# Optimization experiments

Hardware: AMD Instinct MI355X
Metric: run time of the kernel (lower is better)

Reference implementation:

```python
import jax, jax.numpy as jnp
import numpy as np

RADIUS = 0.15
NSAMPLE = 128
NPOINT = 128
EPS = 1e-5  # BatchNorm eps (eval mode, running_mean=0, running_var=1)


def _bn(x, g, b):
    shape = (1, -1) + (1,) * (x.ndim - 2)
    return x * (g / jnp.sqrt(1.0 + EPS)).reshape(shape) + b.reshape(shape)


def _fps(x, npoint):
    # farthest point sampling; x: (Bk, N, 3) -> (Bk, npoint) int32
    Bn, N, _ = x.shape

    def step(carry, _):
        dist, far = carry
        c = jnp.take_along_axis(x, far[:, None, None], 1)  # (Bk,1,3)
        d = jnp.sum((x - c) ** 2, -1)
        dist = jnp.minimum(dist, d)
        return (dist, jnp.argmax(dist, -1).astype(jnp.int32)), far

    init = (jnp.full((Bn, N), 1e10, x.dtype), jnp.zeros((Bn,), jnp.int32))
    _, idxs = jax.lax.scan(step, init, None, length=npoint)
    return idxs.T  # (Bk, npoint)


def _sa_module(x, f, mlp):
    # PointnetSAModuleVotes: FPS -> ball query -> group (use_xyz, normalize_xyz)
    # -> shared MLP (conv2d 1x1 + BN + ReLU) -> max over nsample.
    Bk, M, _ = x.shape
    fps_idx = _fps(x, NPOINT)
    new_xyz = jnp.take_along_axis(x, fps_idx[..., None], 1)  # (Bk,np,3)
    d2 = jnp.sum((new_xyz[:, :, None, :] - x[:, None, :, :]) ** 2, -1)  # (Bk,np,M)
    cand = jnp.where(d2 < RADIUS ** 2, jnp.arange(M)[None, None, :], M)
    cand = jnp.sort(cand, -1)[..., :NSAMPLE]  # first nsample in-radius indices
    first = cand[..., :1]
    first = jnp.where(first == M, 0, first)
    idx = jnp.where(cand == M, first, cand)  # (Bk,np,ns), pad with first valid
    gx = jnp.take_along_axis(x, idx.reshape(Bk, -1)[..., None], 1).reshape(Bk, NPOINT, NSAMPLE, 3)
    gxn = (gx - new_xyz[:, :, None, :]) / RADIUS  # normalize_xyz=True
    gf = jnp.take_along_axis(f[:, :, None, :], idx[:, None, :, :], 3)  # (Bk,C,np,ns)
    h = jnp.concatenate([gxn.transpose(0, 3, 1, 2), gf], 1)  # (Bk, C+3, np, ns)
    for (w, b, g, be) in mlp:
        h = jax.nn.relu(_bn(jnp.einsum('oc,bcps->bops', w, h) + b[None, :, None, None], g, be))
    return new_xyz, h.max(-1)  # (Bk,np,3), (Bk,128,np)


def setup_inputs() -> dict:
    key = jax.random.key(0)
    ks = iter(jax.random.split(key, 40))
    B, M, K, C = 2, 1024, 19, 256
    inp = {}
    inp['xyz'] = jax.random.normal(next(ks), (B, M, K, 3), jnp.float32)
    inp['features'] = jax.random.normal(next(ks), (B, C, K, M), jnp.float32)

    def conv_p(prefix, cin, cout):
        inp[prefix + '_w'] = jax.random.normal(next(ks), (cout, cin), jnp.float32) * (1.0 / np.sqrt(cin))
        inp[prefix + '_b'] = jax.random.normal(next(ks), (cout,), jnp.float32) * 0.02
        inp[prefix + '_g'] = 1.0 + 0.1 * jax.random.normal(next(ks), (cout,), jnp.float32)
        inp[prefix + '_be'] = 0.02 * jax.random.normal(next(ks), (cout,), jnp.float32)

    conv_p('m1', C + 3, 128)  # use_xyz -> 259 in-channels
    conv_p('m2', 128, 128)
    conv_p('m3', 128, 128)
    conv_p('c1', 128, 128)
    conv_p('c2', 128, 128)
    inp['op_w'] = jax.random.normal(next(ks), (K, 5, 128), jnp.float32) * (1.0 / np.sqrt(128))
    inp['op_b'] = jax.random.normal(next(ks), (K, 5), jnp.float32) * 0.02
    return inp


def reference(xyz, features, m1_w, m1_b, m1_g, m1_be, m2_w, m2_b, m2_g, m2_be,
              m3_w, m3_b, m3_g, m3_be, c1_w, c1_b, c1_g, c1_be,
              c2_w, c2_b, c2_g, c2_be, op_w, op_b):
    B, M, K, _ = xyz.shape
    C = features.shape[1]
    # fold vote_factor k into the batch dim (all per-k SA/conv weights are shared)
    x = xyz.transpose(0, 2, 1, 3).reshape(B * K, M, 3)
    f = features.transpose(0, 2, 1, 3).reshape(B * K, C, M)
    mlp = [(m1_w, m1_b, m1_g, m1_be), (m2_w, m2_b, m2_g, m2_be), (m3_w, m3_b, m3_g, m3_be)]
    new_xyz, feat = _sa_module(x, f, mlp)
    net = jax.nn.relu(_bn(jnp.einsum('oc,bcp->bop', c1_w, feat) + c1_b[None, :, None], c1_g, c1_be))
    net = jax.nn.relu(_bn(jnp.einsum('oc,bcp->bop', c2_w, net) + c2_b[None, :, None], c2_g, c2_be))
    net = net.reshape(B, K, 128, NPOINT)
    # per-k output conv (conv_op ModuleList), 128 -> 2+3
    out = jnp.einsum('koc,bkcp->bkop', op_w, net) + op_b[None, :, :, None]
    net_t = out.transpose(0, 1, 3, 2)  # (B,K,np,5)
    agg_xyz = new_xyz.reshape(B, K, NPOINT, 3)
    center = agg_xyz + net_t[..., 2:5]  # decode_scores_
    scores = jnp.concatenate([net_t[..., :2], center], -1)  # obj(2) + center(3)
    return scores, agg_xyz, feat.reshape(B, K, 128, NPOINT)
```

## Files before the change

kernel.cpp:

```cpp
#include <hip/hip_runtime.h>
#include <math.h>

#define NBK   38

#define OFF_XC    0u
#define OFF_NXYZ  466944u
#define OFF_BIDX  525312u
#define OFF_W1F   3015680u
#define OFF_PREP  22938624u
#define OFF_WF    22955008u
#define OFF_CNT   23348224u

#define OUT_AGG   24320
#define OUT_FEAT  38912

typedef short bf16x8 __attribute__((ext_vector_type(8)));
typedef float f32x4  __attribute__((ext_vector_type(4)));
typedef int   v4i    __attribute__((ext_vector_type(4)));
typedef int   v2i    __attribute__((ext_vector_type(2)));

__device__ __forceinline__ float dist2f(float a0, float a1, float a2,
                                        float b0, float b1, float b2) {
#pragma clang fp contract(off)
  float d0 = a0 - b0;
  float d1 = a1 - b1;
  float d2 = a2 - b2;
  return d0 * d0 + d1 * d1 + d2 * d2;
}

__device__ __forceinline__ void split2rn(float v, unsigned& sh, unsigned& sm) {
  unsigned u = __float_as_uint(v);
  unsigned rh = (u + 0x7fffu + ((u >> 16) & 1u)) & 0xffff0000u;
  sh = rh >> 16;
  float r1 = v - __uint_as_float(rh);
  unsigned u1 = __float_as_uint(r1);
  unsigned rm = (u1 + 0x7fffu + ((u1 >> 16) & 1u)) & 0xffff0000u;
  sm = rm >> 16;
}

__global__ __launch_bounds__(1024, 4) void front_kernel(
    const float* __restrict__ xyz, const float* __restrict__ feats,
    const float* __restrict__ m1w, const float* __restrict__ m1b,
    const float* __restrict__ m1g, const float* __restrict__ m1be,
    const float* __restrict__ m2w, const float* __restrict__ m2b,
    const float* __restrict__ m2g, const float* __restrict__ m2be,
    const float* __restrict__ m3w, const float* __restrict__ m3b,
    const float* __restrict__ m3g, const float* __restrict__ m3be,
    const float* __restrict__ c1w, const float* __restrict__ c1b,
    const float* __restrict__ c1g, const float* __restrict__ c1be,
    const float* __restrict__ c2w, const float* __restrict__ c2b,
    const float* __restrict__ c2g, const float* __restrict__ c2be,
    float* __restrict__ xc, float* __restrict__ nxyz, float* __restrict__ agg,
    int* __restrict__ bidx, int* __restrict__ counts,
    float* __restrict__ W1f, short* __restrict__ Wf, float* __restrict__ prep)
{
  __shared__ __align__(16) char smem[32768];
  int bid = blockIdx.x, t = threadIdx.x;
  int wave = t >> 6, lane = t & 63;

  if (bid < NBK) {
    int bk = bid;
    int b = bk / 19, k = bk % 19;
    float* sx0 = (float*)smem;
    float* sx1 = sx0 + 1024;
    float* sx2 = sx1 + 1024;
    float* sp0 = sx2 + 1024;
    float* sp1 = sp0 + 1088;
    float* sp2 = sp1 + 1088;
    float* scen = sp2 + 1088;

    const float* src = xyz + ((size_t)((b * 1024 + t) * 19 + k)) * 3;
    float x0 = src[0], x1 = src[1], x2 = src[2];
    sx0[t] = x0; sx1[t] = x1; sx2[t] = x2;
    int tp = t + (t >> 4);
    sp0[tp] = x0; sp1[tp] = x1; sp2[tp] = x2;
    xc[(bk * 3 + 0) * 1024 + t] = x0;
    xc[(bk * 3 + 1) * 1024 + t] = x1;
    xc[(bk * 3 + 2) * 1024 + t] = x2;
    __syncthreads();

    if (wave == 0) {
      float px[16], py[16], pz[16], dist[16];
      int base = lane * 17;
#pragma unroll
      for (int j = 0; j < 16; ++j) {
        px[j] = sp0[base + j];
        py[j] = sp1[base + j];
        pz[j] = sp2[base + j];
        dist[j] = 1e10f;
      }
      int far = 0;
      for (int it = 0; it < 128; ++it) {
        int fa = far + (far >> 4);
        float c0 = sp0[fa], c1 = sp1[fa], c2 = sp2[fa];
        if (lane == 0) {
          scen[it * 3 + 0] = c0;
          scen[it * 3 + 1] = c1;
          scen[it * 3 + 2] = c2;
        }
#pragma unroll
        for (int j = 0; j < 16; ++j) {
          float d = dist2f(px[j], py[j], pz[j], c0, c1, c2);
          dist[j] = fminf(dist[j], d);
        }
        float tv[8]; int tj[8];
#pragma unroll
        for (int i = 0; i < 8; ++i) {
          bool L = dist[2 * i] >= dist[2 * i + 1];
          tv[i] = L ? dist[2 * i] : dist[2 * i + 1];
          tj[i] = L ? (2 * i) : (2 * i + 1);
        }
#pragma unroll
        for (int s = 1; s < 8; s <<= 1) {
#pragma unroll
          for (int i = 0; i < 8; i += 2 * s) {
            bool L = tv[i] >= tv[i + s];
            tv[i] = L ? tv[i] : tv[i + s];
            tj[i] = L ? tj[i] : tj[i + s];
          }
        }
        float lmax = tv[0];
        float g = lmax;
#pragma unroll
        for (int off = 1; off <= 32; off <<= 1)
          g = fmaxf(g, __shfl_xor(g, off));
        unsigned long long mk = __ballot(lmax == g);
        int wl = __builtin_ctzll(mk);
        far = __shfl((lane << 4) + tj[0], wl);
      }
    }
    __syncthreads();

    if (t < 384) {
      float v = scen[t];
      nxyz[bk * 384 + t] = v;
      agg[bk * 384 + t]  = v;
    }

    for (int p = wave * 8; p < wave * 8 + 8; ++p) {
      float c0 = scen[p * 3 + 0], c1 = scen[p * 3 + 1], c2 = scen[p * 3 + 2];
      int* outp = bidx + ((size_t)(bk * 128 + p)) * 128;
      int count = 0, first = 0;
      bool got = false;
      for (int ch = 0; ch < 16 && count < 128; ++ch) {
        int m = (ch << 6) + lane;
        float d = dist2f(sx0[m], sx1[m], sx2[m], c0, c1, c2);
        bool flag = d < 0.0225f;
        unsigned long long mask = __ballot(flag);
        if (!got && mask) { first = (ch << 6) + __builtin_ctzll(mask); got = true; }
        int pos = count + (int)__popcll(mask & ((1ull << lane) - 1ull));
        if (flag && pos < 128) outp[pos] = m;
        count += (int)__popcll(mask);
      }
      for (int j = count + lane; j < 128; j += 64) outp[j] = first;
      if (lane == 0) counts[bk * 128 + p] = count > 128 ? 128 : count;
    }
    return;
  }

  if (bid < 342) {
    short* ffrag = (short*)smem;
    if (t >= 256) {
      for (int i = 0; i < 8; ++i) __syncthreads();
      return;
    }
    int blk = bid - NBK;
    int bk = blk >> 3, m0 = (blk & 7) << 7;
    int b = bk / 19, k = bk % 19;
    int quad = lane >> 4, nl = lane & 15;
    int mloc = t & 127, chalf = t >> 7;
    int st_w = mloc >> 4, sl_w = mloc & 15;
    const float* fbase = feats + ((size_t)(b * 4864 + k)) * 1024 + m0 + mloc;

    f32x4 acc[2][8];
#pragma unroll
    for (int oi = 0; oi < 2; ++oi)
#pragma unroll
      for (int st = 0; st < 8; ++st) acc[oi][st] = (f32x4){0.f, 0.f, 0.f, 0.f};

    for (int ch = 0; ch < 4; ++ch) {
      int cbase = ch * 64 + chalf * 32;
#pragma unroll
      for (int g = 0; g < 4; ++g) {
        float v[8];
#pragma unroll
        for (int j = 0; j < 8; ++j)
          v[j] = fbase[(size_t)(cbase + g * 8 + j) * 19456];
        unsigned sh[8], sm[8];
#pragma unroll
        for (int j = 0; j < 8; ++j) split2rn(v[j], sh[j], sm[j]);
        int base = chalf * 4096 + st_w * 512 + (g * 16 + sl_w) * 8;
        v4i ph = {(int)(sh[0] | (sh[1] << 16)), (int)(sh[2] | (sh[3] << 16)),
                  (int)(sh[4] | (sh[5] << 16)), (int)(sh[6] | (sh[7] << 16))};
        *(v4i*)&ffrag[base] = ph;
        v4i pm = {(int)(sm[0] | (sm[1] << 16)), (int)(sm[2] | (sm[3] << 16)),
                  (int)(sm[4] | (sm[5] << 16)), (int)(sm[6] | (sm[7] << 16))};
        *(v4i*)&ffrag[base + 8192] = pm;
      }
      __syncthreads();
#pragma unroll
      for (int kkl = 0; kkl < 2; ++kkl) {
        int kk = ch * 2 + kkl;
        bf16x8 a[2][2];
#pragma unroll
        for (int oi = 0; oi < 2; ++oi) {
          int o_row = (wave * 2 + oi) * 16 + nl;
          const float* wsrc = m1w + o_row * 259 + 3 + kk * 32 + quad * 8;
          float wv[8];
#pragma unroll
          for (int j = 0; j < 8; ++j) wv[j] = wsrc[j];
          unsigned sh[8], sm[8];
#pragma unroll
          for (int j = 0; j < 8; ++j) split2rn(wv[j], sh[j], sm[j]);
          short ah[8], am[8];
#pragma unroll
          for (int j = 0; j < 8; ++j) { ah[j] = (short)sh[j]; am[j] = (short)sm[j]; }
          a[oi][0] = (bf16x8){ah[0], ah[1], ah[2], ah[3], ah[4], ah[5], ah[6], ah[7]};
          a[oi][1] = (bf16x8){am[0], am[1], am[2], am[3], am[4], am[5], am[6], am[7]};
        }
#pragma unroll
        for (int st = 0; st < 8; ++st) {
          const short* hb = ffrag + kkl * 4096 + st * 512 + lane * 8;
          bf16x8 b0 = *(const bf16x8*)hb;
          bf16x8 b1 = *(const bf16x8*)(hb + 8192);
#pragma unroll
          for (int oi = 0; oi < 2; ++oi) {
            f32x4 c = acc[oi][st];
            c = __builtin_amdgcn_mfma_f32_16x16x32_bf16(a[oi][1], b0, c, 0, 0, 0);
            c = __builtin_amdgcn_mfma_f32_16x16x32_bf16(a[oi][0], b1, c, 0, 0, 0);
            c = __builtin_amdgcn_mfma_f32_16x16x32_bf16(a[oi][0], b0, c, 0, 0, 0);
            acc[oi][st] = c;
          }
        }
      }
      __syncthreads();
    }
    float inv = 1.0f / sqrtf(1.0f + 1e-5f);
#pragma unroll
    for (int oi = 0; oi < 2; ++oi) {
      int o0 = (wave * 2 + oi) * 16 + quad * 4;
      float4 bb = *(const float4*)&m1b[o0];
      float4 gg = *(const float4*)&m1g[o0];
#pragma unroll
      for (int st = 0; st < 8; ++st) {
        int m_out = m0 + st * 16 + nl;
        f32x4 cc = acc[oi][st];
        float4 r;
        r.x = (cc[0] + bb.x) * (gg.x * inv);
        r.y = (cc[1] + bb.y) * (gg.y * inv);
        r.z = (cc[2] + bb.z) * (gg.z * inv);
        r.w = (cc[3] + bb.w) * (gg.w * inv);
        *(float4*)&W1f[((size_t)(bk * 1024 + m_out)) * 128 + o0] = r;
      }
    }
    return;
  }

  if (bid < 350) {
    int idx = (bid - 342) * 1024 + t;
#pragma unroll
    for (int e = 0; e < 4; ++e) {
      int i = idx * 4 + e;
      int c = i & 127, o = (i >> 7) & 127, l = i >> 14;
      float w = (l ? m3w : m2w)[o * 128 + c];
      unsigned sh, sm;
      split2rn(w, sh, sm);
      int ot = o >> 4, mm = o & 15, kk = c >> 5, q = (c & 31) >> 3, j = c & 7;
      int within = (q * 16 + mm) * 8 + j;
      Wf[(((l * 2 + 0) * 4 + kk) * 8 + ot) * 512 + within] = (short)sh;
      Wf[(((l * 2 + 1) * 4 + kk) * 8 + ot) * 512 + within] = (short)sm;
    }
    return;
  }

  if (bid < 358) {
    int idx2 = (bid - 350) * 1024 + t;
#pragma unroll
    for (int e = 0; e < 4; ++e) {
      int i = idx2 * 4 + e;
      int c = i & 127, o = (i >> 7) & 127, l = i >> 14;
      float w = (l ? c2w : c1w)[o * 128 + c];
      unsigned sh, sm;
      split2rn(w, sh, sm);
      int ot = o >> 4, mm = o & 15, kk = c >> 5, q = (c & 31) >> 3, j = c & 7;
      int within = (q * 16 + mm) * 8 + j;
      Wf[131072 + (((l * 2 + 0) * 4 + kk) * 8 + ot) * 512 + within] = (short)sh;
      Wf[131072 + (((l * 2 + 1) * 4 + kk) * 8 + ot) * 512 + within] = (short)sm;
    }
    return;
  }

  if (t < 128) {
    float inv = 1.0f / sqrtf(1.0f + 1e-5f);
    float a1 = m1g[t] * inv;
    prep[t] = a1;
    float a2 = m2g[t] * inv;  prep[256 + t] = a2;  prep[384 + t] = fmaf(m2b[t], a2, m2be[t]);
    float a3 = m3g[t] * inv;  prep[512 + t] = a3;  prep[640 + t] = fmaf(m3b[t], a3, m3be[t]);
    float ac1 = c1g[t] * inv; prep[768 + t] = ac1; prep[896 + t] = fmaf(c1b[t], ac1, c1be[t]);
    float ac2 = c2g[t] * inv; prep[1024 + t] = ac2; prep[1152 + t] = fmaf(c2b[t], ac2, c2be[t]);
    prep[1280 + 4 * t + 0] = m1w[t * 259 + 0] * a1;
    prep[1280 + 4 * t + 1] = m1w[t * 259 + 1] * a1;
    prep[1280 + 4 * t + 2] = m1w[t * 259 + 2] * a1;
    prep[1280 + 4 * t + 3] = m1be[t];
  }
}

__device__ __forceinline__ void mfma_layer(const short* __restrict__ Wf,
                                           const short* hfrag, int l,
                                           int wave, int lane, int nst_h,
                                           f32x4 acc[2][4])
{
#pragma unroll 1
  for (int kk = 0; kk < 4; ++kk) {
    bf16x8 a[2][2];
#pragma unroll
    for (int oi = 0; oi < 2; ++oi)
#pragma unroll
      for (int sp = 0; sp < 2; ++sp)
        a[oi][sp] = *(const bf16x8*)(Wf + (((l * 2 + sp) * 4 + kk) * 8 + (wave * 2 + oi)) * 512 + lane * 8);
    for (int st = 0; st < nst_h; ++st) {
      const short* hb = hfrag + kk * 2048 + st * 512 + lane * 8;
      bf16x8 b0 = *(const bf16x8*)(hb);
      bf16x8 b1 = *(const bf16x8*)(hb + 8192);
#pragma unroll
      for (int oi = 0; oi < 2; ++oi) {
        f32x4 c = acc[oi][st];
        c = __builtin_amdgcn_mfma_f32_16x16x32_bf16(a[oi][1], b0, c, 0, 0, 0);
        c = __builtin_amdgcn_mfma_f32_16x16x32_bf16(a[oi][0], b1, c, 0, 0, 0);
        c = __builtin_amdgcn_mfma_f32_16x16x32_bf16(a[oi][0], b0, c, 0, 0, 0);
        acc[oi][st] = c;
      }
    }
  }
}

__global__ __launch_bounds__(256, 3) void sa_kernel(
    const float* __restrict__ xc, const float* __restrict__ nxyz,
    const int* __restrict__ bidx, const int* __restrict__ counts,
    const float* __restrict__ W1f, const float* __restrict__ prep,
    const short* __restrict__ Wf, float* __restrict__ feat_out)
{
  __shared__ __align__(16) short hfrag[16384];
  __shared__ float pcs[512];
  __shared__ float sm[32 * 128];
  __shared__ float ccen[12];
  __shared__ int scnt[4];
  int gb = blockIdx.x, bk = gb >> 5, pb = (gb & 31) << 2;
  int t = threadIdx.x;
  int wave = t >> 6, lane = t & 63;
  int quad = lane >> 4, nl = lane & 15;

  pcs[t] = prep[1280 + t];
  pcs[256 + t] = prep[1536 + t];
  if (t < 4) scnt[t] = counts[bk * 128 + pb + t];
  if (t < 12) {
    int bb = t / 3, c = t % 3;
    ccen[t] = nxyz[(bk * 128 + pb + bb) * 3 + c];
  }
  __syncthreads();
  int n0 = (scnt[0] + 15) >> 4, n1 = (scnt[1] + 15) >> 4;
  int n2 = (scnt[2] + 15) >> 4, n3 = (scnt[3] + 15) >> 4;
  int pf1 = n0, pf2 = n0 + n1, pf3 = n0 + n1 + n2, T = n0 + n1 + n2 + n3;

  for (int q0 = 0; q0 < T; q0 += 4) {
    int nst_h = T - q0;
    if (nst_h > 4) nst_h = 4;
    {
      int cg = wave;
      int st = lane >> 4, sl = lane & 15;
      if (st < nst_h) {
        int q = q0 + st;
        int bq = (q >= pf1) + (q >= pf2) + (q >= pf3);
        int tstart = (bq == 0) ? 0 : (bq == 1) ? pf1 : (bq == 2) ? pf2 : pf3;
        int tslot = q - tstart;
        int m = bidx[((size_t)(bk * 128 + pb + bq)) * 128 + tslot * 16 + sl];
        float cen0 = ccen[bq * 3 + 0], cen1 = ccen[bq * 3 + 1], cen2 = ccen[bq * 3 + 2];
        float g0 = (xc[(bk * 3 + 0) * 1024 + m] - cen0) * (1.0f / 0.15f);
        float g1 = (xc[(bk * 3 + 1) * 1024 + m] - cen1) * (1.0f / 0.15f);
        float g2 = (xc[(bk * 3 + 2) * 1024 + m] - cen2) * (1.0f / 0.15f);
        const float4* wrow = (const float4*)(W1f + ((size_t)(bk * 1024 + m)) * 128 + cg * 32);
        const float4* pcp = (const float4*)pcs + cg * 32;
#pragma unroll
        for (int g = 0; g < 4; ++g) {
          float4 wva = wrow[g * 2], wvb = wrow[g * 2 + 1];
          float wv[8] = {wva.x, wva.y, wva.z, wva.w, wvb.x, wvb.y, wvb.z, wvb.w};
          unsigned sh[8], smv[8];
#pragma unroll
          for (int e = 0; e < 8; ++e) {
            float4 pc = pcp[g * 8 + e];
            float hv = fmaxf(wv[e] + pc.x * g0 + pc.y * g1 + pc.z * g2 + pc.w, 0.f);
            split2rn(hv, sh[e], smv[e]);
          }
          int base = (cg * 4 + st) * 512 + (g * 16 + sl) * 8;
          v4i ph = {(int)(sh[0] | (sh[1] << 16)), (int)(sh[2] | (sh[3] << 16)),
                    (int)(sh[4] | (sh[5] << 16)), (int)(sh[6] | (sh[7] << 16))};
          *(v4i*)&hfrag[base] = ph;
          v4i pm = {(int)(smv[0] | (smv[1] << 16)), (int)(smv[2] | (smv[3] << 16)),
                    (int)(smv[4] | (smv[5] << 16)), (int)(smv[6] | (smv[7] << 16))};
          *(v4i*)&hfrag[base + 8192] = pm;
        }
      }
    }
    __syncthreads();

    f32x4 acc[2][4];
#pragma unroll
    for (int oi = 0; oi < 2; ++oi)
#pragma unroll
      for (int st = 0; st < 4; ++st) acc[oi][st] = (f32x4){0.f, 0.f, 0.f, 0.f};
    mfma_layer(Wf, hfrag, 0, wave, lane, nst_h, acc);
    __syncthreads();

#pragma unroll
    for (int oi = 0; oi < 2; ++oi) {
      int o0 = (wave * 2 + oi) * 16 + quad * 4;
      float4 al = *(const float4*)&prep[256 + o0];
      float4 be = *(const float4*)&prep[384 + o0];
      int kk2 = o0 >> 5, g2 = (o0 & 31) >> 3, j0 = o0 & 7;
      for (int st = 0; st < nst_h; ++st) {
        f32x4 cc = acc[oi][st];
        float v0 = fmaxf(fmaf(cc[0], al.x, be.x), 0.f);
        float v1 = fmaxf(fmaf(cc[1], al.y, be.y), 0.f);
        float v2 = fmaxf(fmaf(cc[2], al.z, be.z), 0.f);
        float v3 = fmaxf(fmaf(cc[3], al.w, be.w), 0.f);
        unsigned h0, m0_, h1, m1_, h2, m2_, h3, m3_;
        split2rn(v0, h0, m0_); split2rn(v1, h1, m1_);
        split2rn(v2, h2, m2_); split2rn(v3, h3, m3_);
        int base = (kk2 * 4 + st) * 512 + (g2 * 16 + nl) * 8 + j0;
        v2i w0 = {(int)(h0 | (h1 << 16)), (int)(h2 | (h3 << 16))};
        *(v2i*)&hfrag[base] = w0;
        v2i w1 = {(int)(m0_ | (m1_ << 16)), (int)(m2_ | (m3_ << 16))};
        *(v2i*)&hfrag[base + 8192] = w1;
      }
    }
    __syncthreads();

#pragma unroll
    for (int oi = 0; oi < 2; ++oi)
#pragma unroll
      for (int st = 0; st < 4; ++st) acc[oi][st] = (f32x4){0.f, 0.f, 0.f, 0.f};
    mfma_layer(Wf, hfrag, 1, wave, lane, nst_h, acc);

#pragma unroll
    for (int oi = 0; oi < 2; ++oi) {
      int o0 = (wave * 2 + oi) * 16 + quad * 4;
      float4 al = *(const float4*)&prep[512 + o0];
      float4 be = *(const float4*)&prep[640 + o0];
      for (int st = 0; st < nst_h; ++st) {
        f32x4 cc = acc[oi][st];
        float v[4];
        v[0] = fmaxf(fmaf(cc[0], al.x, be.x), 0.f);
        v[1] = fmaxf(fmaf(cc[1], al.y, be.y), 0.f);
        v[2] = fmaxf(fmaf(cc[2], al.z, be.z), 0.f);
        v[3] = fmaxf(fmaf(cc[3], al.w, be.w), 0.f);
#pragma unroll
        for (int r = 0; r < 4; ++r) {
          float x = v[r];
          x = fmaxf(x, __shfl_xor(x, 1));
          x = fmaxf(x, __shfl_xor(x, 2));
          x = fmaxf(x, __shfl_xor(x, 4));
          x = fmaxf(x, __shfl_xor(x, 8));
          if (nl == 0) sm[(q0 + st) * 128 + o0 + r] = x;
        }
      }
    }
    __syncthreads();
  }

#pragma unroll
  for (int e = t; e < 512; e += 256) {
    int bb = e >> 7, o = e & 127;
    int qs = (bb == 0) ? 0 : (bb == 1) ? pf1 : (bb == 2) ? pf2 : pf3;
    int nq = (bb == 0) ? n0 : (bb == 1) ? n1 : (bb == 2) ? n2 : n3;
    float v = sm[qs * 128 + o];
    for (int q = 1; q < nq; ++q) v = fmaxf(v, sm[(qs + q) * 128 + o]);
    feat_out[(((size_t)bk) << 14) + (o << 7) + pb + bb] = v;
  }
}

__global__ __launch_bounds__(256) void head_kernel(const float* __restrict__ featg,
    const float* __restrict__ prep, const short* __restrict__ Wf,
    const float* __restrict__ nxyz, const float* __restrict__ opw,
    const float* __restrict__ opb, float* __restrict__ scores)
{
  __shared__ __align__(16) short hfrag[16384];
  __shared__ float hplain[128 * 65];
  int bk = blockIdx.x >> 1, p0 = (blockIdx.x & 1) << 6;
  int t = threadIdx.x;
  int wave = t >> 6, lane = t & 63;
  int quad = lane >> 4, nl = lane & 15;
  const short* WC = Wf + 131072;

  {
    int cg = wave;
    int st = lane >> 4, sl = lane & 15;
    const float* fb = featg + (bk << 14) + p0 + lane;
#pragma unroll
    for (int g = 0; g < 4; ++g) {
      float v[8];
#pragma unroll
      for (int e = 0; e < 8; ++e)
        v[e] = fb[(cg * 32 + g * 8 + e) << 7];
      unsigned sh[8], sm[8];
#pragma unroll
      for (int e = 0; e < 8; ++e) split2rn(v[e], sh[e], sm[e]);
      int base = (cg * 4 + st) * 512 + (g * 16 + sl) * 8;
      v4i ph = {(int)(sh[0] | (sh[1] << 16)), (int)(sh[2] | (sh[3] << 16)),
                (int)(sh[4] | (sh[5] << 16)), (int)(sh[6] | (sh[7] << 16))};
      *(v4i*)&hfrag[base] = ph;
      v4i pm = {(int)(sm[0] | (sm[1] << 16)), (int)(sm[2] | (sm[3] << 16)),
                (int)(sm[4] | (sm[5] << 16)), (int)(sm[6] | (sm[7] << 16))};
      *(v4i*)&hfrag[base + 8192] = pm;
    }
  }
  __syncthreads();

  f32x4 acc[2][4];
#pragma unroll
  for (int oi = 0; oi < 2; ++oi)
#pragma unroll
    for (int st = 0; st < 4; ++st) acc[oi][st] = (f32x4){0.f, 0.f, 0.f, 0.f};
  mfma_layer(WC, hfrag, 0, wave, lane, 4, acc);
  __syncthreads();

#pragma unroll
  for (int oi = 0; oi < 2; ++oi) {
    int o0 = (wave * 2 + oi) * 16 + quad * 4;
    float4 al = *(const float4*)&prep[768 + o0];
    float4 be = *(const float4*)&prep[896 + o0];
    int kk2 = o0 >> 5, g2 = (o0 & 31) >> 3, j0 = o0 & 7;
#pragma unroll
    for (int st = 0; st < 4; ++st) {
      f32x4 cc = acc[oi][st];
      float v0 = fmaxf(fmaf(cc[0], al.x, be.x), 0.f);
      float v1 = fmaxf(fmaf(cc[1], al.y, be.y), 0.f);
      float v2 = fmaxf(fmaf(cc[2], al.z, be.z), 0.f);
      float v3 = fmaxf(fmaf(cc[3], al.w, be.w), 0.f);
      unsigned h0, m0_, h1, m1_, h2, m2_, h3, m3_;
      split2rn(v0, h0, m0_); split2rn(v1, h1, m1_);
      split2rn(v2, h2, m2_); split2rn(v3, h3, m3_);
      int base = (kk2 * 4 + st) * 512 + (g2 * 16 + nl) * 8 + j0;
      v2i w0 = {(int)(h0 | (h1 << 16)), (int)(h2 | (h3 << 16))};
      *(v2i*)&hfrag[base] = w0;
      v2i w1 = {(int)(m0_ | (m1_ << 16)), (int)(m2_ | (m3_ << 16))};
      *(v2i*)&hfrag[base + 8192] = w1;
    }
  }
  __syncthreads();

#pragma unroll
  for (int oi = 0; oi < 2; ++oi)
#pragma unroll
    for (int st = 0; st < 4; ++st) acc[oi][st] = (f32x4){0.f, 0.f, 0.f, 0.f};
  mfma_layer(WC, hfrag, 1, wave, lane, 4, acc);

#pragma unroll
  for (int oi = 0; oi < 2; ++oi) {
    int o0 = (wave * 2 + oi) * 16 + quad * 4;
    float4 al = *(const float4*)&prep[1024 + o0];
    float4 be = *(const float4*)&prep[1152 + o0];
#pragma unroll
    for (int st = 0; st < 4; ++st) {
      f32x4 cc = acc[oi][st];
      int p = st * 16 + nl;
      hplain[(o0 + 0) * 65 + p] = fmaxf(fmaf(cc[0], al.x, be.x), 0.f);
      hplain[(o0 + 1) * 65 + p] = fmaxf(fmaf(cc[1], al.y, be.y), 0.f);
      hplain[(o0 + 2) * 65 + p] = fmaxf(fmaf(cc[2], al.z, be.z), 0.f);
      hplain[(o0 + 3) * 65 + p] = fmaxf(fmaf(cc[3], al.w, be.w), 0.f);
    }
  }
  __syncthreads();

  if (t < 64) {
    int p = t, k = bk % 19;
    float res[5];
#pragma unroll
    for (int j = 0; j < 5; ++j) {
      const float* wr = opw + ((size_t)(k * 5 + j)) * 128;
      float a = opb[k * 5 + j];
      for (int c = 0; c < 128; ++c) a = fmaf(wr[c], hplain[c * 65 + p], a);
      res[j] = a;
    }
    int pg = p0 + p;
    float a0 = nxyz[(bk * 128 + pg) * 3 + 0];
    float a1 = nxyz[(bk * 128 + pg) * 3 + 1];
    float a2 = nxyz[(bk * 128 + pg) * 3 + 2];
    float* sc = scores + ((size_t)(bk * 128 + pg)) * 5;
    sc[0] = res[0];
    sc[1] = res[1];
    sc[2] = a0 + res[2];
    sc[3] = a1 + res[3];
    sc[4] = a2 + res[4];
  }
}

extern "C" void kernel_launch(void* const* d_in, const int* in_sizes, int n_in,
                              void* d_out, int out_size, void* d_ws, size_t ws_size,
                              hipStream_t stream) {
  (void)in_sizes; (void)n_in; (void)out_size; (void)ws_size;
  const float* xyz  = (const float*)d_in[0];
  const float* fts  = (const float*)d_in[1];
  const float* m1w  = (const float*)d_in[2];
  const float* m1b  = (const float*)d_in[3];
  const float* m1g  = (const float*)d_in[4];
  const float* m1be = (const float*)d_in[5];
  const float* m2w  = (const float*)d_in[6];
  const float* m2b  = (const float*)d_in[7];
  const float* m2g  = (const float*)d_in[8];
  const float* m2be = (const float*)d_in[9];
  const float* m3w  = (const float*)d_in[10];
  const float* m3b  = (const float*)d_in[11];
  const float* m3g  = (const float*)d_in[12];
  const float* m3be = (const float*)d_in[13];
  const float* c1w  = (const float*)d_in[14];
  const float* c1b  = (const float*)d_in[15];
  const float* c1g  = (const float*)d_in[16];
  const float* c1be = (const float*)d_in[17];
  const float* c2w  = (const float*)d_in[18];
  const float* c2b  = (const float*)d_in[19];
  const float* c2g  = (const float*)d_in[20];
  const float* c2be = (const float*)d_in[21];
  const float* opw  = (const float*)d_in[22];
  const float* opb  = (const float*)d_in[23];

  float* out = (float*)d_out;
  char* ws = (char*)d_ws;
  float* xc   = (float*)(ws + OFF_XC);
  float* nxyz = (float*)(ws + OFF_NXYZ);
  int*   bidx = (int*)(ws + OFF_BIDX);
  float* W1f  = (float*)(ws + OFF_W1F);
  float* prep = (float*)(ws + OFF_PREP);
  short* Wf   = (short*)(ws + OFF_WF);
  int*   cnt  = (int*)(ws + OFF_CNT);

  hipLaunchKernelGGL(front_kernel, dim3(359), dim3(1024), 0, stream,
                     xyz, fts, m1w, m1b, m1g, m1be, m2w, m2b, m2g, m2be,
                     m3w, m3b, m3g, m3be, c1w, c1b, c1g, c1be,
                     c2w, c2b, c2g, c2be,
                     xc, nxyz, out + OUT_AGG, bidx, cnt, W1f, Wf, prep);
  hipLaunchKernelGGL(sa_kernel, dim3(NBK * 32), dim3(256), 0, stream,
                     xc, nxyz, bidx, cnt, W1f, prep, Wf, out + OUT_FEAT);
  hipLaunchKernelGGL(head_kernel, dim3(NBK * 2), dim3(256), 0, stream,
                     out + OUT_FEAT, prep, Wf, nxyz, opw, opb, out);
}
```

Baseline: 295.4 us.

## Speed up FPS loop with DPP max reduction, float4 LDS points, 512-thread blocks

The serial farthest-point-sampling loop now finds the wave-wide maximum with DPP row reductions plus four readlanes, instead of a six-step shfl_xor butterfly. The per-point index is fetched with readlane rather than a shuffle. Point coordinates move to a single float4-per-point LDS array, so each centre or point is read with one 16-byte load. The front kernel drops to 512-thread blocks, so ball query covers 16 centres per wave and the weight-splitting blocks are doubled to keep the same coverage. The aim is to shorten the latency-bound single-wave FPS critical path, at the cost of fewer threads doing the grouping work in parallel.

```diff
diff --git a/kernel.cpp b/kernel.cpp
--- a/kernel.cpp
+++ b/kernel.cpp
@@ -38,7 +38,14 @@
   sm = rm >> 16;
 }
 
-__global__ __launch_bounds__(1024, 4) void front_kernel(
+#define DPP_FMAX_STEP(v, ctrl)                                                 \
+  {                                                                            \
+    int _s = __builtin_amdgcn_update_dpp(__float_as_int(v), __float_as_int(v), \
+                                         (ctrl), 0xf, 0xf, false);             \
+    (v) = fmaxf((v), __int_as_float(_s));                                      \
+  }
+
+__global__ __launch_bounds__(512, 2) void front_kernel(
     const float* __restrict__ xyz, const float* __restrict__ feats,
     const float* __restrict__ m1w, const float* __restrict__ m1b,
     const float* __restrict__ m1g, const float* __restrict__ m1be,
@@ -61,46 +68,38 @@
   if (bid < NBK) {
     int bk = bid;
     int b = bk / 19, k = bk % 19;
-    float* sx0 = (float*)smem;
-    float* sx1 = sx0 + 1024;
-    float* sx2 = sx1 + 1024;
-    float* sp0 = sx2 + 1024;
-    float* sp1 = sp0 + 1088;
-    float* sp2 = sp1 + 1088;
-    float* scen = sp2 + 1088;
-
-    const float* src = xyz + ((size_t)((b * 1024 + t) * 19 + k)) * 3;
-    float x0 = src[0], x1 = src[1], x2 = src[2];
-    sx0[t] = x0; sx1[t] = x1; sx2[t] = x2;
-    int tp = t + (t >> 4);
-    sp0[tp] = x0; sp1[tp] = x1; sp2[tp] = x2;
-    xc[(bk * 3 + 0) * 1024 + t] = x0;
-    xc[(bk * 3 + 1) * 1024 + t] = x1;
-    xc[(bk * 3 + 2) * 1024 + t] = x2;
+    float4* sp4 = (float4*)smem;
+    float4* scen4 = (float4*)(smem + 16384);
+
+    for (int i = t; i < 1024; i += 512) {
+      const float* src = xyz + ((size_t)((b * 1024 + i) * 19 + k)) * 3;
+      float x0 = src[0], x1 = src[1], x2 = src[2];
+      sp4[i] = make_float4(x0, x1, x2, 0.f);
+      xc[(bk * 3 + 0) * 1024 + i] = x0;
+      xc[(bk * 3 + 1) * 1024 + i] = x1;
+      xc[(bk * 3 + 2) * 1024 + i] = x2;
+    }
     __syncthreads();
 
     if (wave == 0) {
       float px[16], py[16], pz[16], dist[16];
-      int base = lane * 17;
 #pragma unroll
       for (int j = 0; j < 16; ++j) {
-        px[j] = sp0[base + j];
-        py[j] = sp1[base + j];
-        pz[j] = sp2[base + j];
+        float4 p = sp4[(lane << 4) + j];
+        px[j] = p.x; py[j] = p.y; pz[j] = p.z;
         dist[j] = 1e10f;
       }
+#pragma unroll
+      for (int j = 0; j < 16; ++j)
+        asm volatile("" : "+v"(px[j]), "+v"(py[j]), "+v"(pz[j]));
+
       int far = 0;
       for (int it = 0; it < 128; ++it) {
-        int fa = far + (far >> 4);
-        float c0 = sp0[fa], c1 = sp1[fa], c2 = sp2[fa];
-        if (lane == 0) {
-          scen[it * 3 + 0] = c0;
-          scen[it * 3 + 1] = c1;
-          scen[it * 3 + 2] = c2;
-        }
+        float4 c = sp4[far];
+        if (lane == 0) scen4[it] = c;
 #pragma unroll
         for (int j = 0; j < 16; ++j) {
-          float d = dist2f(px[j], py[j], pz[j], c0, c1, c2);
+          float d = dist2f(px[j], py[j], pz[j], c.x, c.y, c.z);
           dist[j] = fminf(dist[j], d);
         }
         float tv[8]; int tj[8];
@@ -121,30 +120,37 @@
         }
         float lmax = tv[0];
         float g = lmax;
-#pragma unroll
-        for (int off = 1; off <= 32; off <<= 1)
-          g = fmaxf(g, __shfl_xor(g, off));
-        unsigned long long mk = __ballot(lmax == g);
-        int wl = __builtin_ctzll(mk);
-        far = __shfl((lane << 4) + tj[0], wl);
+        DPP_FMAX_STEP(g, 0x111);
+        DPP_FMAX_STEP(g, 0x112);
+        DPP_FMAX_STEP(g, 0x114);
+        DPP_FMAX_STEP(g, 0x118);
+        float r0 = __int_as_float(__builtin_amdgcn_readlane(__float_as_int(g), 15));
+        float r1 = __int_as_float(__builtin_amdgcn_readlane(__float_as_int(g), 31));
+        float r2 = __int_as_float(__builtin_amdgcn_readlane(__float_as_int(g), 47));
+        float r3 = __int_as_float(__builtin_amdgcn_readlane(__float_as_int(g), 63));
+        float gmax = fmaxf(fmaxf(r0, r1), fmaxf(r2, r3));
+        unsigned long long mk = __ballot(lmax == gmax);
+        int wl = (int)__builtin_ctzll(mk);
+        far = __builtin_amdgcn_readlane((lane << 4) + tj[0], wl);
       }
     }
     __syncthreads();
 
     if (t < 384) {
-      float v = scen[t];
+      float v = ((const float*)scen4)[(t / 3) * 4 + (t % 3)];
       nxyz[bk * 384 + t] = v;
       agg[bk * 384 + t]  = v;
     }
 
-    for (int p = wave * 8; p < wave * 8 + 8; ++p) {
-      float c0 = scen[p * 3 + 0], c1 = scen[p * 3 + 1], c2 = scen[p * 3 + 2];
+    for (int p = wave * 16; p < wave * 16 + 16; ++p) {
+      float4 cen = scen4[p];
       int* outp = bidx + ((size_t)(bk * 128 + p)) * 128;
       int count = 0, first = 0;
       bool got = false;
       for (int ch = 0; ch < 16 && count < 128; ++ch) {
         int m = (ch << 6) + lane;
-        float d = dist2f(sx0[m], sx1[m], sx2[m], c0, c1, c2);
+        float4 pv = sp4[m];
+        float d = dist2f(pv.x, pv.y, pv.z, cen.x, cen.y, cen.z);
         bool flag = d < 0.0225f;
         unsigned long long mask = __ballot(flag);
         if (!got && mask) { first = (ch << 6) + __builtin_ctzll(mask); got = true; }
@@ -256,8 +262,8 @@
     return;
   }
 
-  if (bid < 350) {
-    int idx = (bid - 342) * 1024 + t;
+  if (bid < 358) {
+    int idx = (bid - 342) * 512 + t;
 #pragma unroll
     for (int e = 0; e < 4; ++e) {
       int i = idx * 4 + e;
@@ -273,8 +279,8 @@
     return;
   }
 
-  if (bid < 358) {
-    int idx2 = (bid - 350) * 1024 + t;
+  if (bid < 374) {
+    int idx2 = (bid - 358) * 512 + t;
 #pragma unroll
     for (int e = 0; e < 4; ++e) {
       int i = idx2 * 4 + e;
@@ -633,7 +639,7 @@
   short* Wf   = (short*)(ws + OFF_WF);
   int*   cnt  = (int*)(ws + OFF_CNT);
 
-  hipLaunchKernelGGL(front_kernel, dim3(359), dim3(1024), 0, stream,
+  hipLaunchKernelGGL(front_kernel, dim3(375), dim3(512), 0, stream,
                      xyz, fts, m1w, m1b, m1g, m1be, m2w, m2b, m2g, m2be,
                      m3w, m3b, m3g, m3be, c1w, c1b, c1g, c1be,
                      c2w, c2b, c2g, c2be,
```

New measurement: 297.6 us. No clear change (+0.7%).
